# Kernel optimization log

Measured on AMD Instinct MI355X. Metric: run time of the kernel, lower is better.

The kernel has to match this reference:

```python
import jax, jax.numpy as jnp
import numpy as np
import math

EMBED_DIM = 1024
N_HEADS = 16
HEAD_DIM = EMBED_DIM // N_HEADS
NUM_FEATURES = 32
R_NODES = 2
EPS = 1e-06
C_CONST = 2.0 + EPS
CHUNK = 512


def setup_inputs() -> dict:
    key = jax.random.key(0)
    ks = jax.random.split(key, 8)
    B, T = 2, 4096
    x = jax.random.normal(ks[0], (B, T, EMBED_DIM), dtype=jnp.float32)
    w_qkv = jax.random.normal(ks[1], (3 * EMBED_DIM, EMBED_DIM), dtype=jnp.float32) * 0.02
    b_qkv = jnp.zeros((3 * EMBED_DIM,), dtype=jnp.float32)
    w_out = jax.random.normal(ks[2], (EMBED_DIM, EMBED_DIM), dtype=jnp.float32) * 0.02
    b_out = jnp.zeros((EMBED_DIM,), dtype=jnp.float32)
    omega = jax.random.normal(ks[3], (R_NODES, N_HEADS, HEAD_DIM, NUM_FEATURES), dtype=jnp.float32)
    nodes, weights = np.polynomial.laguerre.laggauss(R_NODES)
    quad_nodes = jnp.asarray(nodes, dtype=jnp.float32) / C_CONST
    quad_weights = jnp.asarray(weights, dtype=jnp.float32) / C_CONST
    return {"x": x, "w_qkv": w_qkv, "b_qkv": b_qkv, "w_out": w_out,
            "b_out": b_out, "omega": omega, "quad_nodes": quad_nodes,
            "quad_weights": quad_weights}


def _compute_features(z, omega, quad_nodes, quad_weights):
    # z: [B,H,T,D] -> fused features [B,H,T,R*M]
    R, M = omega.shape[0], omega.shape[-1]
    nrm = jnp.linalg.norm(z, axis=-1, keepdims=True)
    zn = z / jnp.maximum(nrm, 1e-12)  # F.normalize
    proj = jnp.einsum('bhtd,rhdm->rbhtm', zn, omega)
    inv_sqrt_m = 1.0 / math.sqrt(M)
    poly = (proj ** 2) * inv_sqrt_m
    s = quad_nodes.reshape(R, 1, 1, 1, 1)
    sqrt_2s = jnp.sqrt(2.0 * jnp.maximum(quad_nodes, 0.0)).reshape(R, 1, 1, 1, 1)
    exp_arg = jnp.clip(proj * sqrt_2s - s, -20.0, 20.0)
    prf = jnp.exp(exp_arg) * inv_sqrt_m
    sqw = jnp.sqrt(jnp.maximum(quad_weights, 0.0)).reshape(R, 1, 1, 1, 1)
    fused = poly * prf * sqw  # [R,B,H,T,M]
    B, H, T = z.shape[0], z.shape[1], z.shape[2]
    return jnp.transpose(fused, (1, 2, 3, 0, 4)).reshape(B, H, T, R * M)


def _forward(x, w_qkv, b_qkv, w_out, b_out, omega, quad_nodes, quad_weights):
    B, T, C = x.shape
    H, D = N_HEADS, HEAD_DIM
    qkv = x @ w_qkv.T + b_qkv  # [B,T,3C]
    q, k, v = jnp.split(qkv, 3, axis=-1)
    def to_bhtd(t):
        return jnp.transpose(t.reshape(B, T, H, D), (0, 2, 1, 3)).astype(jnp.float32)
    q, k, v = to_bhtd(q), to_bhtd(k), to_bhtd(v)
    qf = _compute_features(q, omega, quad_nodes, quad_weights)  # [B,H,T,F]
    kf = _compute_features(k, omega, quad_nodes, quad_weights)
    F_dim = qf.shape[-1]
    nc = T // CHUNK
    # chunked causal linear attention via scan over chunks
    def to_chunks(t):  # [B,H,T,...] -> [nc,B,H,CHUNK,...]
        new_shape = (t.shape[0], t.shape[1], nc, CHUNK) + t.shape[3:]
        return jnp.moveaxis(t.reshape(new_shape), 2, 0)
    qf_c, kf_c, v_c = to_chunks(qf), to_chunks(kf), to_chunks(v)

    kv0 = jnp.zeros((B, H, F_dim, D), dtype=jnp.float32)
    k0 = jnp.zeros((B, H, F_dim), dtype=jnp.float32)

    def step(carry, inp):
        kv_s, k_s = carry
        qc, kc, vc = inp
        kv_prod = jnp.einsum('bhtf,bhtd->bhtfd', kc, vc)
        kv_cum = jnp.cumsum(kv_prod, axis=2) + kv_s[:, :, None]
        k_cum = jnp.cumsum(kc, axis=2) + k_s[:, :, None]
        ctx = jnp.einsum('bhtf,bhtfd->bhtd', qc, kv_cum)
        den = jnp.maximum(jnp.einsum('bhtf,bhtf->bht', qc, k_cum), 1e-06)
        out_c = ctx / den[..., None]
        return (kv_cum[:, :, -1], k_cum[:, :, -1]), out_c

    _, out_chunks = jax.lax.scan(step, (kv0, k0), (qf_c, kf_c, v_c))
    out = jnp.moveaxis(out_chunks, 0, 2).reshape(B, H, T, D)  # [B,H,T,D]
    out = jnp.transpose(out, (0, 2, 1, 3)).reshape(B, T, C)
    return out @ w_out.T + b_out


def reference(x, w_qkv, b_qkv, w_out, b_out, omega, quad_nodes, quad_weights):
    return _forward(x, w_qkv, b_qkv, w_out, b_out, omega, quad_nodes, quad_weights)
```

## Files before the change

kernel.cpp:

```cpp
#include <hip/hip_runtime.h>
#include <math.h>

#define EMBED   1024
#define THREEC  3072
#define NH      16
#define HD      64
#define NFEAT   64
#define RN      2
#define MM_     32
#define B_      2
#define T_      4096
#define L_      64
#define NC_     64
#define BH_     32

typedef __attribute__((ext_vector_type(8))) short bf16x8;
typedef __attribute__((ext_vector_type(4))) float f32x4;

__device__ __forceinline__ float bf2f(short s) {
    unsigned u = ((unsigned)(unsigned short)s) << 16;
    return __builtin_bit_cast(float, u);
}
__device__ __forceinline__ short f2bf(float f) {
    unsigned u = __builtin_bit_cast(unsigned, f);
    u += 0x7fff + ((u >> 16) & 1);
    return (short)(u >> 16);
}
__device__ __forceinline__ void gload16(const short* g, short* l) {
    __builtin_amdgcn_global_load_lds(
        (const __attribute__((address_space(1))) void*)g,
        (__attribute__((address_space(3))) void*)l, 16, 0, 0);
}

#define NV_X   1048576
#define NV_WQ  393216
#define NV_WO  131072
#define NV_ALL (NV_X + NV_WQ + NV_WO)
__global__ __launch_bounds__(256) void prep_kernel(
    const float* __restrict__ x, const float* __restrict__ wq,
    const float* __restrict__ wo, const float* __restrict__ omega,
    short* __restrict__ xb, short* __restrict__ wqb, short* __restrict__ wob,
    short* __restrict__ omgH, short* __restrict__ omgL)
{
    int i = blockIdx.x * 256 + threadIdx.x;
    if (i < NV_ALL) {
        const float* src; short* dst; int k;
        if (i < NV_X)            { src = x;  dst = xb;  k = i; }
        else if (i < NV_X+NV_WQ) { src = wq; dst = wqb; k = i - NV_X; }
        else                     { src = wo; dst = wob; k = i - NV_X - NV_WQ; }
        const float4* p = (const float4*)src + (size_t)k * 2;
        float4 a = p[0], b = p[1];
        bf16x8 o = { f2bf(a.x), f2bf(a.y), f2bf(a.z), f2bf(a.w),
                     f2bf(b.x), f2bf(b.y), f2bf(b.z), f2bf(b.w) };
        *((bf16x8*)dst + k) = o;
    } else {
        int j = i - NV_ALL;
        if (j < NH * NFEAT * HD) {
            int d = j & 63;
            int f = (j >> 6) & 63;
            int h = j >> 12;
            int r = f >> 5, m = f & 31;
            float w = omega[(((size_t)(r * NH + h) * HD + d) * MM_) + m];
            short a = f2bf(w);
            omgH[j] = a;
            omgL[j] = f2bf(w - bf2f(a));
        }
    }
}

template<int OUTBF>
__global__ __launch_bounds__(256) void gemm_bf16(
    const short* __restrict__ A,
    const short* __restrict__ W,
    const float* __restrict__ bias,
    float* __restrict__ Cf, short* __restrict__ Cb,
    int M, int N, int K)
{
    __shared__ short lA[2][128 * 32];
    __shared__ short lB[2][128 * 32];
    const int tid  = threadIdx.x;
    const int bm   = blockIdx.y * 128;
    const int bn   = blockIdx.x * 128;
    const int lane = tid & 63;
    const int wave = tid >> 6;
    const int row0 = (wave >> 1) * 64;
    const int col0 = (wave & 1) * 64;
    const int lr   = lane & 15;
    const int kg8  = (lane >> 4) * 8;

    f32x4 acc[4][4] = {};

#define STAGE(buf, k0)                                                        \
    {                                                                         \
        _Pragma("unroll")                                                     \
        for (int i = 0; i < 2; ++i) {                                         \
            int idx = i * 256 + tid;                                          \
            int row = idx >> 2, kq = (idx & 3) * 8;                           \
            gload16(&A[(size_t)(bm + row) * K + (k0) + kq], &lA[buf][idx * 8]); \
            gload16(&W[(size_t)(bn + row) * K + (k0) + kq], &lB[buf][idx * 8]); \
        }                                                                     \
    }

    const int KT = K >> 5;
    STAGE(0, 0);
    __syncthreads();
    int cur = 0;
    for (int kt = 0; kt < KT; ++kt) {
        if (kt + 1 < KT) STAGE(cur ^ 1, (kt + 1) * 32);
        const short* As = lA[cur];
        const short* Bs = lB[cur];
        bf16x8 af[4], bfr[4];
        #pragma unroll
        for (int m = 0; m < 4; ++m)
            af[m] = *(const bf16x8*)&As[(row0 + m * 16 + lr) * 32 + kg8];
        #pragma unroll
        for (int n = 0; n < 4; ++n)
            bfr[n] = *(const bf16x8*)&Bs[(col0 + n * 16 + lr) * 32 + kg8];
        #pragma unroll
        for (int m = 0; m < 4; ++m)
            #pragma unroll
            for (int n = 0; n < 4; ++n)
                acc[m][n] = __builtin_amdgcn_mfma_f32_16x16x32_bf16(
                    af[m], bfr[n], acc[m][n], 0, 0, 0);
        __syncthreads();
        cur ^= 1;
    }
#undef STAGE

    #pragma unroll
    for (int n = 0; n < 4; ++n) {
        const int col = bn + col0 + n * 16 + (lane & 15);
        const float bvv = bias[col];
        #pragma unroll
        for (int m = 0; m < 4; ++m) {
            const int rbase = bm + row0 + m * 16 + (lane >> 4) * 4;
            #pragma unroll
            for (int j = 0; j < 4; ++j) {
                const float v = acc[m][n][j] + bvv;
                if (OUTBF) Cb[(size_t)(rbase + j) * N + col] = f2bf(v);
                else       Cf[(size_t)(rbase + j) * N + col] = v;
            }
        }
    }
}

__global__ __launch_bounds__(256) void features_chunk(
    const short* __restrict__ qkvb,
    const short* __restrict__ omgH,
    const short* __restrict__ omgL,
    const float* __restrict__ qn,
    const float* __restrict__ qw,
    short* __restrict__ qf,
    short* __restrict__ kf,
    float* __restrict__ cKV,
    float* __restrict__ cK)
{
    __shared__ short zq[64][72];
    __shared__ short zk[64][72];
    __shared__ short omh[64][72];
    __shared__ short oml[64][72];
    __shared__ float invn[2][64];

    const int tid   = threadIdx.x;
    const int chunk = blockIdx.x;
    const int bh    = chunk >> 6;
    const int c     = chunk & 63;
    const int b     = bh >> 4, h = bh & 15;
    const int t0    = c * 64;

    {
        const int row = tid >> 2;
        const int c0  = (tid & 3) * 16;
        const size_t zbase = ((size_t)(b * T_ + t0 + row)) * THREEC + h * HD + c0;
        const size_t obase = ((size_t)h * NFEAT + row) * HD + c0;
        *(bf16x8*)&zq[row][c0]      = *(const bf16x8*)&qkvb[zbase];
        *(bf16x8*)&zq[row][c0 + 8]  = *(const bf16x8*)&qkvb[zbase + 8];
        *(bf16x8*)&zk[row][c0]      = *(const bf16x8*)&qkvb[zbase + EMBED];
        *(bf16x8*)&zk[row][c0 + 8]  = *(const bf16x8*)&qkvb[zbase + EMBED + 8];
        *(bf16x8*)&omh[row][c0]     = *(const bf16x8*)&omgH[obase];
        *(bf16x8*)&omh[row][c0 + 8] = *(const bf16x8*)&omgH[obase + 8];
        *(bf16x8*)&oml[row][c0]     = *(const bf16x8*)&omgL[obase];
        *(bf16x8*)&oml[row][c0 + 8] = *(const bf16x8*)&omgL[obase + 8];
    }
    __syncthreads();

    {
        const int t = tid >> 2;
        const int q = tid & 3;
        #pragma unroll
        for (int p = 0; p < 2; ++p) {
            const short* Z = p ? &zk[t][q * 16] : &zq[t][q * 16];
            float ss = 0.0f;
            #pragma unroll
            for (int j = 0; j < 16; ++j) { float v = bf2f(Z[j]); ss += v * v; }
            ss += __shfl_xor(ss, 1, 64);
            ss += __shfl_xor(ss, 2, 64);
            if (q == 0) invn[p][t] = 1.0f / fmaxf(sqrtf(ss), 1e-12f);
        }
    }
    __syncthreads();

    const int wave = tid >> 6;
    const int lane = tid & 63;
    const int p    = wave >> 1;
    const int half = wave & 1;
    const short (*Z)[72] = p ? zk : zq;

    const float s0 = qn[0], s1 = qn[1];
    const float sq2s0 = sqrtf(2.0f * fmaxf(s0, 0.0f));
    const float sq2s1 = sqrtf(2.0f * fmaxf(s1, 0.0f));
    const float sc0 = sqrtf(fmaxf(qw[0], 0.0f)) * (1.0f / 32.0f);
    const float sc1 = sqrtf(fmaxf(qw[1], 0.0f)) * (1.0f / 32.0f);

    const int lr  = lane & 15;
    const int G   = lane >> 4;
    const int kg8 = G * 8;

    f32x4 acc[2][4] = {};
    #pragma unroll
    for (int kk = 0; kk < 2; ++kk) {
        bf16x8 a[2], bh8[4], bl8[4];
        #pragma unroll
        for (int m = 0; m < 2; ++m)
            a[m] = *(const bf16x8*)&Z[half * 32 + m * 16 + lr][kk * 32 + kg8];
        #pragma unroll
        for (int n = 0; n < 4; ++n) {
            bh8[n] = *(const bf16x8*)&omh[n * 16 + lr][kk * 32 + kg8];
            bl8[n] = *(const bf16x8*)&oml[n * 16 + lr][kk * 32 + kg8];
        }
        #pragma unroll
        for (int m = 0; m < 2; ++m)
            #pragma unroll
            for (int n = 0; n < 4; ++n) {
                acc[m][n] = __builtin_amdgcn_mfma_f32_16x16x32_bf16(
                    a[m], bh8[n], acc[m][n], 0, 0, 0);
                acc[m][n] = __builtin_amdgcn_mfma_f32_16x16x32_bf16(
                    a[m], bl8[n], acc[m][n], 0, 0, 0);
            }
    }
    __syncthreads();

    short (*kfT)[72] = zq;
    short (*vT)[72]  = zk;
    {
        short* dstbase = (p ? kf : qf) + ((size_t)bh * T_ + t0) * NFEAT;
        #pragma unroll
        for (int n = 0; n < 4; ++n) {
            const int f = n * 16 + lr;
            const float s_r   = (n < 2) ? s0 : s1;
            const float sq2s  = (n < 2) ? sq2s0 : sq2s1;
            const float scale = (n < 2) ? sc0 : sc1;
            #pragma unroll
            for (int m = 0; m < 2; ++m) {
                const int tb4 = half * 32 + m * 16 + G * 4;
                #pragma unroll
                for (int j = 0; j < 4; ++j) {
                    const int t = tb4 + j;
                    const float proj = acc[m][n][j] * invn[p][t];
                    const float arg = fminf(fmaxf(proj * sq2s - s_r, -20.0f), 20.0f);
                    const float val = proj * proj * __expf(arg) * scale;
                    const short vb  = f2bf(val);
                    dstbase[(size_t)t * NFEAT + f] = vb;
                    if (p == 1) kfT[f][t] = vb;
                }
            }
        }
    }
    {
        const int row = tid >> 2;
        const int c0  = (tid & 3) * 16;
        const short* vrow = qkvb + ((size_t)(b * T_ + t0 + row)) * THREEC
                          + 2 * EMBED + h * HD;
        bf16x8 v0 = *(const bf16x8*)&vrow[c0], v1 = *(const bf16x8*)&vrow[c0 + 8];
        #pragma unroll
        for (int j = 0; j < 8; ++j) {
            vT[c0 + j][row]     = v0[j];
            vT[c0 + 8 + j][row] = v1[j];
        }
    }
    __syncthreads();

    {
        bf16x8 a2[2], bv8[4][2];
        a2[0] = *(const bf16x8*)&kfT[wave * 16 + lr][kg8];
        a2[1] = *(const bf16x8*)&kfT[wave * 16 + lr][32 + kg8];
        #pragma unroll
        for (int n = 0; n < 4; ++n) {
            bv8[n][0] = *(const bf16x8*)&vT[n * 16 + lr][kg8];
            bv8[n][1] = *(const bf16x8*)&vT[n * 16 + lr][32 + kg8];
        }
        f32x4 sa[4] = {};
        #pragma unroll
        for (int n = 0; n < 4; ++n) {
            sa[n] = __builtin_amdgcn_mfma_f32_16x16x32_bf16(a2[0], bv8[n][0], sa[n], 0, 0, 0);
            sa[n] = __builtin_amdgcn_mfma_f32_16x16x32_bf16(a2[1], bv8[n][1], sa[n], 0, 0, 0);
        }
        float* base = cKV + (size_t)chunk * (NFEAT * HD);
        #pragma unroll
        for (int n = 0; n < 4; ++n) {
            float4 o; o.x = sa[n][0]; o.y = sa[n][1]; o.z = sa[n][2]; o.w = sa[n][3];
            *(float4*)&base[(n * 16 + lr) * NFEAT + wave * 16 + G * 4] = o;
        }
    }
    {
        const int f  = tid >> 2;
        const int tq = tid & 3;
        float s = 0.0f;
        #pragma unroll
        for (int j = 0; j < 16; ++j) s += bf2f(kfT[f][tq * 16 + j]);
        s += __shfl_xor(s, 1, 64);
        s += __shfl_xor(s, 2, 64);
        if (tq == 0) cK[(size_t)chunk * NFEAT + f] = s;
    }
}

__global__ __launch_bounds__(256) void prefix_scan(
    float* __restrict__ cKV, float* __restrict__ cK)
{
    const int bh  = blockIdx.x >> 2;
    const int sl  = blockIdx.x & 3;
    const int tid = threadIdx.x;
    float4* base = (float4*)(cKV + (size_t)bh * NC_ * (NFEAT * HD) + sl * 1024) + tid;
    float4 n0 = base[0];
    float4 n1 = base[1024];
    float4 pref; pref.x = pref.y = pref.z = pref.w = 0.0f;
    for (int c = 0; c < NC_; ++c) {
        float4 cur = n0;
        n0 = n1;
        if (c + 2 < NC_) n1 = base[(size_t)(c + 2) * 1024];
        else { n1.x = n1.y = n1.z = n1.w = 0.0f; }
        base[(size_t)c * 1024] = pref;
        pref.x += cur.x; pref.y += cur.y; pref.z += cur.z; pref.w += cur.w;
    }
    if (sl == 0 && tid < 64) {
        float* kb = cK + (size_t)bh * NC_ * NFEAT + tid;
        float m0 = kb[0];
        float m1 = kb[64];
        float p = 0.0f;
        for (int c = 0; c < NC_; ++c) {
            float cu = m0;
            m0 = m1;
            m1 = (c + 2 < NC_) ? kb[(size_t)(c + 2) * 64] : 0.0f;
            kb[(size_t)c * 64] = p;
            p += cu;
        }
    }
}

__global__ __launch_bounds__(256) void intra_mfma(
    const short* __restrict__ qf,
    const short* __restrict__ kf,
    const short* __restrict__ qkvb,
    const float* __restrict__ cKV,
    const float* __restrict__ cK,
    short* __restrict__ attnb)
{
    __shared__ short Qs[64][72];
    __shared__ short Ks[64][72];
    __shared__ short Vt[64][72];
    __shared__ short Pp[64][72];
    __shared__ short At[64][72];
    __shared__ float rs_l[64], qkp_l[64], cKp[64];

    const int tid = threadIdx.x;
    const int chunk = blockIdx.x;
    const int bh = chunk >> 6, c = chunk & 63;
    const int b = bh >> 4, h = bh & 15;
    const int t0 = c * L_;

    {
        const int row = tid >> 2;
        const int c0  = (tid & 3) * 16;
        const short* qrow = qf + ((size_t)bh * T_ + t0 + row) * NFEAT;
        const short* krow = kf + ((size_t)bh * T_ + t0 + row) * NFEAT;
        const short* vrow = qkvb + ((size_t)(b * T_ + t0 + row)) * THREEC + 2 * EMBED + h * HD;
        *(bf16x8*)&Qs[row][c0]     = *(const bf16x8*)&qrow[c0];
        *(bf16x8*)&Qs[row][c0 + 8] = *(const bf16x8*)&qrow[c0 + 8];
        *(bf16x8*)&Ks[row][c0]     = *(const bf16x8*)&krow[c0];
        *(bf16x8*)&Ks[row][c0 + 8] = *(const bf16x8*)&krow[c0 + 8];
        bf16x8 v0 = *(const bf16x8*)&vrow[c0], v1 = *(const bf16x8*)&vrow[c0 + 8];
        #pragma unroll
        for (int j = 0; j < 8; ++j) {
            Vt[c0 + j][row]     = v0[j];
            Vt[c0 + 8 + j][row] = v1[j];
        }
        const float* pbase = cKV + (size_t)chunk * (NFEAT * HD) + tid * 16;
        float4 p0 = *(const float4*)&pbase[0],  p1 = *(const float4*)&pbase[4];
        float4 p2 = *(const float4*)&pbase[8],  p3 = *(const float4*)&pbase[12];
        bf16x8 o0 = { f2bf(p0.x), f2bf(p0.y), f2bf(p0.z), f2bf(p0.w),
                      f2bf(p1.x), f2bf(p1.y), f2bf(p1.z), f2bf(p1.w) };
        bf16x8 o1 = { f2bf(p2.x), f2bf(p2.y), f2bf(p2.z), f2bf(p2.w),
                      f2bf(p3.x), f2bf(p3.y), f2bf(p3.z), f2bf(p3.w) };
        *(bf16x8*)&Pp[row][c0]     = o0;
        *(bf16x8*)&Pp[row][c0 + 8] = o1;
        if (tid < 64) cKp[tid] = cK[(size_t)chunk * NFEAT + tid];
    }
    __syncthreads();

    const int wave = tid >> 6;
    const int lane = tid & 63;
    const int lr   = lane & 15;
    const int kg   = (lane >> 4) * 8;
    const int r0   = wave * 16;

    bf16x8 aq[2];
    aq[0] = *(const bf16x8*)&Qs[r0 + lr][kg];
    aq[1] = *(const bf16x8*)&Qs[r0 + lr][32 + kg];
    f32x4 accA[4] = {};
    #pragma unroll
    for (int n = 0; n < 4; ++n) {
        accA[n] = __builtin_amdgcn_mfma_f32_16x16x32_bf16(
            aq[0], *(const bf16x8*)&Ks[n * 16 + lr][kg], accA[n], 0, 0, 0);
        accA[n] = __builtin_amdgcn_mfma_f32_16x16x32_bf16(
            aq[1], *(const bf16x8*)&Ks[n * 16 + lr][32 + kg], accA[n], 0, 0, 0);
    }
    float rsum[4] = {0.0f, 0.0f, 0.0f, 0.0f};
    #pragma unroll
    for (int n = 0; n < 4; ++n) {
        const int s = n * 16 + lr;
        #pragma unroll
        for (int j = 0; j < 4; ++j) {
            const int t = r0 + (lane >> 4) * 4 + j;
            const float a = (s <= t) ? accA[n][j] : 0.0f;
            rsum[j] += a;
            At[t][s] = f2bf(a);
        }
    }
    #pragma unroll
    for (int j = 0; j < 4; ++j) {
        rsum[j] += __shfl_xor(rsum[j], 1, 64);
        rsum[j] += __shfl_xor(rsum[j], 2, 64);
        rsum[j] += __shfl_xor(rsum[j], 4, 64);
        rsum[j] += __shfl_xor(rsum[j], 8, 64);
    }
    if (lr == 0) {
        #pragma unroll
        for (int j = 0; j < 4; ++j) rs_l[r0 + (lane >> 4) * 4 + j] = rsum[j];
    }

    {
        const int t  = tid >> 2;
        const int fq = (tid & 3) * 16;
        float s = 0.0f;
        #pragma unroll
        for (int j = 0; j < 16; ++j) s += bf2f(Qs[t][fq + j]) * cKp[fq + j];
        s += __shfl_xor(s, 1, 64);
        s += __shfl_xor(s, 2, 64);
        if ((tid & 3) == 0) qkp_l[t] = s;
    }
    __syncthreads();

    bf16x8 aa[2];
    aa[0] = *(const bf16x8*)&At[r0 + lr][kg];
    aa[1] = *(const bf16x8*)&At[r0 + lr][32 + kg];
    f32x4 acc[4] = {};
    #pragma unroll
    for (int n = 0; n < 4; ++n) {
        acc[n] = __builtin_amdgcn_mfma_f32_16x16x32_bf16(
            aa[0], *(const bf16x8*)&Vt[n * 16 + lr][kg], acc[n], 0, 0, 0);
        acc[n] = __builtin_amdgcn_mfma_f32_16x16x32_bf16(
            aa[1], *(const bf16x8*)&Vt[n * 16 + lr][32 + kg], acc[n], 0, 0, 0);
        acc[n] = __builtin_amdgcn_mfma_f32_16x16x32_bf16(
            aq[0], *(const bf16x8*)&Pp[n * 16 + lr][kg], acc[n], 0, 0, 0);
        acc[n] = __builtin_amdgcn_mfma_f32_16x16x32_bf16(
            aq[1], *(const bf16x8*)&Pp[n * 16 + lr][32 + kg], acc[n], 0, 0, 0);
    }

    float inv[4];
    #pragma unroll
    for (int j = 0; j < 4; ++j) {
        const int t = r0 + (lane >> 4) * 4 + j;
        inv[j] = 1.0f / fmaxf(rs_l[t] + qkp_l[t], 1e-6f);
    }
    #pragma unroll
    for (int n = 0; n < 4; ++n) {
        const int d = n * 16 + lr;
        #pragma unroll
        for (int j = 0; j < 4; ++j) {
            const int t = r0 + (lane >> 4) * 4 + j;
            attnb[((size_t)(b * T_ + t0 + t)) * EMBED + h * HD + d] =
                f2bf(acc[n][j] * inv[j]);
        }
    }
}

extern "C" void kernel_launch(void* const* d_in, const int* in_sizes, int n_in,
                              void* d_out, int out_size, void* d_ws, size_t ws_size,
                              hipStream_t stream)
{
    const float* x     = (const float*)d_in[0];
    const float* w_qkv = (const float*)d_in[1];
    const float* b_qkv = (const float*)d_in[2];
    const float* w_out = (const float*)d_in[3];
    const float* b_out = (const float*)d_in[4];
    const float* omega = (const float*)d_in[5];
    const float* qn    = (const float*)d_in[6];
    const float* qw    = (const float*)d_in[7];
    float* out = (float*)d_out;

    short* xb    = (short*)d_ws;
    short* wqb   = xb    + 8388608;
    short* wob   = wqb   + 3145728;
    short* qkvb  = wob   + 1048576;
    short* attnb = qkvb  + 25165824;
    short* omgH  = attnb + 8388608;
    short* omgL  = omgH  + 65536;
    short* qfb   = omgL  + 65536;
    short* kfb   = qfb   + 8388608;
    float* cKV   = (float*)(kfb + 8388608);
    float* cK    = cKV + 8388608;

    const int M = B_ * T_;

    prep_kernel<<<dim3((NV_ALL + 65536) / 256), 256, 0, stream>>>(
        x, w_qkv, w_out, omega, xb, wqb, wob, omgH, omgL);

    gemm_bf16<1><<<dim3(THREEC / 128, M / 128), 256, 0, stream>>>(
        xb, wqb, b_qkv, nullptr, qkvb, M, THREEC, EMBED);
    features_chunk<<<dim3(BH_ * NC_), 256, 0, stream>>>(
        qkvb, omgH, omgL, qn, qw, qfb, kfb, cKV, cK);
    prefix_scan<<<dim3(BH_ * 4), 256, 0, stream>>>(cKV, cK);
    intra_mfma<<<dim3(BH_ * NC_), 256, 0, stream>>>(qfb, kfb, qkvb, cKV, cK, attnb);
    gemm_bf16<0><<<dim3(EMBED / 128, M / 128), 256, 0, stream>>>(
        attnb, wob, b_out, out, nullptr, M, EMBED, EMBED);
}
```

Measured before the change: 170.7 us.

## Fuse intra-chunk attention into feature kernel and store chunk KV states in bf16

Intra-chunk causal attention (QK^T mask, A·V and row sums) now runs inside the features kernel, which already holds the Q/K features and V in shared memory. The partial context and row sums go to global memory, and the inter-chunk kernel only applies the prefix state and normalises. This drops the kf write and reread plus the V reload. Per-chunk KV states and their prefix sums are now stored in bf16 instead of fp32, halving that traffic at some precision cost in the prefix accumulation. An extra bf16 ctx buffer is written and read, which adds traffic and rounds the intra-chunk context once more.

```diff
diff --git a/kernel.cpp b/kernel.cpp
--- a/kernel.cpp
+++ b/kernel.cpp
@@ -15,6 +15,7 @@
 #define BH_     32
 
 typedef __attribute__((ext_vector_type(8))) short bf16x8;
+typedef __attribute__((ext_vector_type(4))) short bf16x4;
 typedef __attribute__((ext_vector_type(4))) float f32x4;
 
 __device__ __forceinline__ float bf2f(short s) {
@@ -144,15 +145,16 @@
     }
 }
 
-__global__ __launch_bounds__(256) void features_chunk(
+__global__ __launch_bounds__(256) void feat_fused(
     const short* __restrict__ qkvb,
     const short* __restrict__ omgH,
     const short* __restrict__ omgL,
     const float* __restrict__ qn,
     const float* __restrict__ qw,
     short* __restrict__ qf,
-    short* __restrict__ kf,
-    float* __restrict__ cKV,
+    short* __restrict__ ctxb,
+    float* __restrict__ rs_g,
+    short* __restrict__ cKVb,
     float* __restrict__ cK)
 {
     __shared__ short zq[64][72];
@@ -160,6 +162,7 @@
     __shared__ short omh[64][72];
     __shared__ short oml[64][72];
     __shared__ float invn[2][64];
+    __shared__ float rs_l[64];
 
     const int tid   = threadIdx.x;
     const int chunk = blockIdx.x;
@@ -242,8 +245,9 @@
 
     short (*kfT)[72] = zq;
     short (*vT)[72]  = zk;
-    {
-        short* dstbase = (p ? kf : qf) + ((size_t)bh * T_ + t0) * NFEAT;
+    short (*Qrm)[72] = omh;
+    short (*Krm)[72] = oml;
+    {
         #pragma unroll
         for (int n = 0; n < 4; ++n) {
             const int f = n * 16 + lr;
@@ -260,8 +264,8 @@
                     const float arg = fminf(fmaxf(proj * sq2s - s_r, -20.0f), 20.0f);
                     const float val = proj * proj * __expf(arg) * scale;
                     const short vb  = f2bf(val);
-                    dstbase[(size_t)t * NFEAT + f] = vb;
-                    if (p == 1) kfT[f][t] = vb;
+                    if (p == 0) { Qrm[t][f] = vb; }
+                    else        { kfT[f][t] = vb; Krm[t][f] = vb; }
                 }
             }
         }
@@ -280,26 +284,67 @@
     }
     __syncthreads();
 
-    {
-        bf16x8 a2[2], bv8[4][2];
+    const int r0 = wave * 16;
+
+    {
+        const int row = tid >> 2;
+        const int c0  = (tid & 3) * 16;
+        short* dst = qf + ((size_t)bh * T_ + t0 + row) * NFEAT;
+        *(bf16x8*)&dst[c0]     = *(const bf16x8*)&Qrm[row][c0];
+        *(bf16x8*)&dst[c0 + 8] = *(const bf16x8*)&Qrm[row][c0 + 8];
+    }
+    bf16x8 aqq[2];
+    aqq[0] = *(const bf16x8*)&Qrm[r0 + lr][kg8];
+    aqq[1] = *(const bf16x8*)&Qrm[r0 + lr][32 + kg8];
+    f32x4 accA[4] = {};
+    #pragma unroll
+    for (int n = 0; n < 4; ++n) {
+        accA[n] = __builtin_amdgcn_mfma_f32_16x16x32_bf16(
+            aqq[0], *(const bf16x8*)&Krm[n * 16 + lr][kg8], accA[n], 0, 0, 0);
+        accA[n] = __builtin_amdgcn_mfma_f32_16x16x32_bf16(
+            aqq[1], *(const bf16x8*)&Krm[n * 16 + lr][32 + kg8], accA[n], 0, 0, 0);
+    }
+    {
+        float rsum[4] = {0.0f, 0.0f, 0.0f, 0.0f};
+        #pragma unroll
+        for (int n = 0; n < 4; ++n) {
+            const int s = n * 16 + lr;
+            #pragma unroll
+            for (int j = 0; j < 4; ++j) {
+                const int t = r0 + G * 4 + j;
+                if (s <= t) rsum[j] += accA[n][j];
+            }
+        }
+        #pragma unroll
+        for (int j = 0; j < 4; ++j) {
+            rsum[j] += __shfl_xor(rsum[j], 1, 64);
+            rsum[j] += __shfl_xor(rsum[j], 2, 64);
+            rsum[j] += __shfl_xor(rsum[j], 4, 64);
+            rsum[j] += __shfl_xor(rsum[j], 8, 64);
+        }
+        if (lr == 0) {
+            #pragma unroll
+            for (int j = 0; j < 4; ++j) rs_l[r0 + G * 4 + j] = rsum[j];
+        }
+    }
+    {
+        bf16x8 a2[2];
         a2[0] = *(const bf16x8*)&kfT[wave * 16 + lr][kg8];
         a2[1] = *(const bf16x8*)&kfT[wave * 16 + lr][32 + kg8];
-        #pragma unroll
-        for (int n = 0; n < 4; ++n) {
-            bv8[n][0] = *(const bf16x8*)&vT[n * 16 + lr][kg8];
-            bv8[n][1] = *(const bf16x8*)&vT[n * 16 + lr][32 + kg8];
-        }
         f32x4 sa[4] = {};
         #pragma unroll
         for (int n = 0; n < 4; ++n) {
-            sa[n] = __builtin_amdgcn_mfma_f32_16x16x32_bf16(a2[0], bv8[n][0], sa[n], 0, 0, 0);
-            sa[n] = __builtin_amdgcn_mfma_f32_16x16x32_bf16(a2[1], bv8[n][1], sa[n], 0, 0, 0);
-        }
-        float* base = cKV + (size_t)chunk * (NFEAT * HD);
-        #pragma unroll
-        for (int n = 0; n < 4; ++n) {
-            float4 o; o.x = sa[n][0]; o.y = sa[n][1]; o.z = sa[n][2]; o.w = sa[n][3];
-            *(float4*)&base[(n * 16 + lr) * NFEAT + wave * 16 + G * 4] = o;
+            sa[n] = __builtin_amdgcn_mfma_f32_16x16x32_bf16(
+                a2[0], *(const bf16x8*)&vT[n * 16 + lr][kg8], sa[n], 0, 0, 0);
+            sa[n] = __builtin_amdgcn_mfma_f32_16x16x32_bf16(
+                a2[1], *(const bf16x8*)&vT[n * 16 + lr][32 + kg8], sa[n], 0, 0, 0);
+        }
+        short* basep = cKVb + (size_t)chunk * (NFEAT * HD);
+        #pragma unroll
+        for (int n = 0; n < 4; ++n) {
+            bf16x4 o = { f2bf(sa[n][0]), f2bf(sa[n][1]),
+                         f2bf(sa[n][2]), f2bf(sa[n][3]) };
+            *(bf16x4*)&basep[(n * 16 + lr) * NFEAT + wave * 16 + G * 4] = o;
         }
     }
     {
@@ -312,25 +357,64 @@
         s += __shfl_xor(s, 2, 64);
         if (tq == 0) cK[(size_t)chunk * NFEAT + f] = s;
     }
+    __syncthreads();
+
+    short (*At)[72] = oml;
+    #pragma unroll
+    for (int n = 0; n < 4; ++n) {
+        const int s = n * 16 + lr;
+        #pragma unroll
+        for (int j = 0; j < 4; ++j) {
+            const int t = r0 + G * 4 + j;
+            At[t][s] = f2bf((s <= t) ? accA[n][j] : 0.0f);
+        }
+    }
+    __syncthreads();
+
+    {
+        bf16x8 aa[2];
+        aa[0] = *(const bf16x8*)&At[r0 + lr][kg8];
+        aa[1] = *(const bf16x8*)&At[r0 + lr][32 + kg8];
+        f32x4 a2[4] = {};
+        #pragma unroll
+        for (int n = 0; n < 4; ++n) {
+            a2[n] = __builtin_amdgcn_mfma_f32_16x16x32_bf16(
+                aa[0], *(const bf16x8*)&vT[n * 16 + lr][kg8], a2[n], 0, 0, 0);
+            a2[n] = __builtin_amdgcn_mfma_f32_16x16x32_bf16(
+                aa[1], *(const bf16x8*)&vT[n * 16 + lr][32 + kg8], a2[n], 0, 0, 0);
+        }
+        #pragma unroll
+        for (int n = 0; n < 4; ++n) {
+            const int d = n * 16 + lr;
+            #pragma unroll
+            for (int j = 0; j < 4; ++j) {
+                const int t = r0 + G * 4 + j;
+                ctxb[((size_t)bh * T_ + t0 + t) * NFEAT + d] = f2bf(a2[n][j]);
+            }
+        }
+    }
+    if (tid < 64) rs_g[(size_t)bh * T_ + t0 + tid] = rs_l[tid];
 }
 
 __global__ __launch_bounds__(256) void prefix_scan(
-    float* __restrict__ cKV, float* __restrict__ cK)
+    short* __restrict__ cKVb, float* __restrict__ cK)
 {
     const int bh  = blockIdx.x >> 2;
     const int sl  = blockIdx.x & 3;
     const int tid = threadIdx.x;
-    float4* base = (float4*)(cKV + (size_t)bh * NC_ * (NFEAT * HD) + sl * 1024) + tid;
-    float4 n0 = base[0];
-    float4 n1 = base[1024];
-    float4 pref; pref.x = pref.y = pref.z = pref.w = 0.0f;
+    short* base = cKVb + (size_t)bh * NC_ * (NFEAT * HD) + sl * 1024 + tid * 4;
+    bf16x4 n0 = *(const bf16x4*)(base);
+    bf16x4 n1 = *(const bf16x4*)(base + 4096);
+    float pref[4] = {0.0f, 0.0f, 0.0f, 0.0f};
     for (int c = 0; c < NC_; ++c) {
-        float4 cur = n0;
+        bf16x4 cur = n0;
         n0 = n1;
-        if (c + 2 < NC_) n1 = base[(size_t)(c + 2) * 1024];
-        else { n1.x = n1.y = n1.z = n1.w = 0.0f; }
-        base[(size_t)c * 1024] = pref;
-        pref.x += cur.x; pref.y += cur.y; pref.z += cur.z; pref.w += cur.w;
+        if (c + 2 < NC_) n1 = *(const bf16x4*)(base + (size_t)(c + 2) * 4096);
+        else { n1[0] = 0; n1[1] = 0; n1[2] = 0; n1[3] = 0; }
+        bf16x4 o = { f2bf(pref[0]), f2bf(pref[1]), f2bf(pref[2]), f2bf(pref[3]) };
+        *(bf16x4*)(base + (size_t)c * 4096) = o;
+        pref[0] += bf2f(cur[0]); pref[1] += bf2f(cur[1]);
+        pref[2] += bf2f(cur[2]); pref[3] += bf2f(cur[3]);
     }
     if (sl == 0 && tid < 64) {
         float* kb = cK + (size_t)bh * NC_ * NFEAT + tid;
@@ -347,139 +431,86 @@
     }
 }
 
-__global__ __launch_bounds__(256) void intra_mfma(
+__global__ __launch_bounds__(256) void inter_attn(
     const short* __restrict__ qf,
-    const short* __restrict__ kf,
-    const short* __restrict__ qkvb,
-    const float* __restrict__ cKV,
-    const float* __restrict__ cK,
+    const short* __restrict__ ctxb,
+    const float* __restrict__ rs_g,
+    const short* __restrict__ cKVp,
+    const float* __restrict__ cKp_g,
     short* __restrict__ attnb)
 {
-    __shared__ short Qs[64][72];
-    __shared__ short Ks[64][72];
-    __shared__ short Vt[64][72];
+    __shared__ short Q[64][72];
     __shared__ short Pp[64][72];
-    __shared__ short At[64][72];
-    __shared__ float rs_l[64], qkp_l[64], cKp[64];
+    __shared__ float cKp[64], rs[64], qkp_l[64];
 
     const int tid = threadIdx.x;
     const int chunk = blockIdx.x;
     const int bh = chunk >> 6, c = chunk & 63;
     const int b = bh >> 4, h = bh & 15;
-    const int t0 = c * L_;
+    const int t0 = c * 64;
 
     {
         const int row = tid >> 2;
         const int c0  = (tid & 3) * 16;
-        const short* qrow = qf + ((size_t)bh * T_ + t0 + row) * NFEAT;
-        const short* krow = kf + ((size_t)bh * T_ + t0 + row) * NFEAT;
-        const short* vrow = qkvb + ((size_t)(b * T_ + t0 + row)) * THREEC + 2 * EMBED + h * HD;
-        *(bf16x8*)&Qs[row][c0]     = *(const bf16x8*)&qrow[c0];
-        *(bf16x8*)&Qs[row][c0 + 8] = *(const bf16x8*)&qrow[c0 + 8];
-        *(bf16x8*)&Ks[row][c0]     = *(const bf16x8*)&krow[c0];
-        *(bf16x8*)&Ks[row][c0 + 8] = *(const bf16x8*)&krow[c0 + 8];
-        bf16x8 v0 = *(const bf16x8*)&vrow[c0], v1 = *(const bf16x8*)&vrow[c0 + 8];
-        #pragma unroll
-        for (int j = 0; j < 8; ++j) {
-            Vt[c0 + j][row]     = v0[j];
-            Vt[c0 + 8 + j][row] = v1[j];
-        }
-        const float* pbase = cKV + (size_t)chunk * (NFEAT * HD) + tid * 16;
-        float4 p0 = *(const float4*)&pbase[0],  p1 = *(const float4*)&pbase[4];
-        float4 p2 = *(const float4*)&pbase[8],  p3 = *(const float4*)&pbase[12];
-        bf16x8 o0 = { f2bf(p0.x), f2bf(p0.y), f2bf(p0.z), f2bf(p0.w),
-                      f2bf(p1.x), f2bf(p1.y), f2bf(p1.z), f2bf(p1.w) };
-        bf16x8 o1 = { f2bf(p2.x), f2bf(p2.y), f2bf(p2.z), f2bf(p2.w),
-                      f2bf(p3.x), f2bf(p3.y), f2bf(p3.z), f2bf(p3.w) };
-        *(bf16x8*)&Pp[row][c0]     = o0;
-        *(bf16x8*)&Pp[row][c0 + 8] = o1;
-        if (tid < 64) cKp[tid] = cK[(size_t)chunk * NFEAT + tid];
-    }
-    __syncthreads();
-
-    const int wave = tid >> 6;
-    const int lane = tid & 63;
-    const int lr   = lane & 15;
-    const int kg   = (lane >> 4) * 8;
-    const int r0   = wave * 16;
-
-    bf16x8 aq[2];
-    aq[0] = *(const bf16x8*)&Qs[r0 + lr][kg];
-    aq[1] = *(const bf16x8*)&Qs[r0 + lr][32 + kg];
-    f32x4 accA[4] = {};
-    #pragma unroll
-    for (int n = 0; n < 4; ++n) {
-        accA[n] = __builtin_amdgcn_mfma_f32_16x16x32_bf16(
-            aq[0], *(const bf16x8*)&Ks[n * 16 + lr][kg], accA[n], 0, 0, 0);
-        accA[n] = __builtin_amdgcn_mfma_f32_16x16x32_bf16(
-            aq[1], *(const bf16x8*)&Ks[n * 16 + lr][32 + kg], accA[n], 0, 0, 0);
-    }
-    float rsum[4] = {0.0f, 0.0f, 0.0f, 0.0f};
-    #pragma unroll
-    for (int n = 0; n < 4; ++n) {
-        const int s = n * 16 + lr;
-        #pragma unroll
-        for (int j = 0; j < 4; ++j) {
-            const int t = r0 + (lane >> 4) * 4 + j;
-            const float a = (s <= t) ? accA[n][j] : 0.0f;
-            rsum[j] += a;
-            At[t][s] = f2bf(a);
-        }
-    }
-    #pragma unroll
-    for (int j = 0; j < 4; ++j) {
-        rsum[j] += __shfl_xor(rsum[j], 1, 64);
-        rsum[j] += __shfl_xor(rsum[j], 2, 64);
-        rsum[j] += __shfl_xor(rsum[j], 4, 64);
-        rsum[j] += __shfl_xor(rsum[j], 8, 64);
-    }
-    if (lr == 0) {
-        #pragma unroll
-        for (int j = 0; j < 4; ++j) rs_l[r0 + (lane >> 4) * 4 + j] = rsum[j];
-    }
+        const short* qrow = qf   + ((size_t)bh * T_ + t0 + row) * NFEAT;
+        const short* prow = cKVp + (size_t)chunk * (NFEAT * HD) + row * NFEAT;
+        *(bf16x8*)&Q[row][c0]      = *(const bf16x8*)&qrow[c0];
+        *(bf16x8*)&Q[row][c0 + 8]  = *(const bf16x8*)&qrow[c0 + 8];
+        *(bf16x8*)&Pp[row][c0]     = *(const bf16x8*)&prow[c0];
+        *(bf16x8*)&Pp[row][c0 + 8] = *(const bf16x8*)&prow[c0 + 8];
+        if (tid < 64) {
+            cKp[tid] = cKp_g[(size_t)chunk * NFEAT + tid];
+            rs[tid]  = rs_g[(size_t)bh * T_ + t0 + tid];
+        }
+    }
+    __syncthreads();
 
     {
         const int t  = tid >> 2;
         const int fq = (tid & 3) * 16;
         float s = 0.0f;
         #pragma unroll
-        for (int j = 0; j < 16; ++j) s += bf2f(Qs[t][fq + j]) * cKp[fq + j];
+        for (int j = 0; j < 16; ++j) s += bf2f(Q[t][fq + j]) * cKp[fq + j];
         s += __shfl_xor(s, 1, 64);
         s += __shfl_xor(s, 2, 64);
         if ((tid & 3) == 0) qkp_l[t] = s;
     }
-    __syncthreads();
-
-    bf16x8 aa[2];
-    aa[0] = *(const bf16x8*)&At[r0 + lr][kg];
-    aa[1] = *(const bf16x8*)&At[r0 + lr][32 + kg];
+
+    const int wave = tid >> 6;
+    const int lane = tid & 63;
+    const int lr = lane & 15;
+    const int G  = lane >> 4;
+    const int kg = G * 8;
+    const int r0 = wave * 16;
+
+    bf16x8 aq[2];
+    aq[0] = *(const bf16x8*)&Q[r0 + lr][kg];
+    aq[1] = *(const bf16x8*)&Q[r0 + lr][32 + kg];
     f32x4 acc[4] = {};
     #pragma unroll
     for (int n = 0; n < 4; ++n) {
-        acc[n] = __builtin_amdgcn_mfma_f32_16x16x32_bf16(
-            aa[0], *(const bf16x8*)&Vt[n * 16 + lr][kg], acc[n], 0, 0, 0);
-        acc[n] = __builtin_amdgcn_mfma_f32_16x16x32_bf16(
-            aa[1], *(const bf16x8*)&Vt[n * 16 + lr][32 + kg], acc[n], 0, 0, 0);
         acc[n] = __builtin_amdgcn_mfma_f32_16x16x32_bf16(
             aq[0], *(const bf16x8*)&Pp[n * 16 + lr][kg], acc[n], 0, 0, 0);
         acc[n] = __builtin_amdgcn_mfma_f32_16x16x32_bf16(
             aq[1], *(const bf16x8*)&Pp[n * 16 + lr][32 + kg], acc[n], 0, 0, 0);
     }
+    __syncthreads();
 
     float inv[4];
     #pragma unroll
     for (int j = 0; j < 4; ++j) {
-        const int t = r0 + (lane >> 4) * 4 + j;
-        inv[j] = 1.0f / fmaxf(rs_l[t] + qkp_l[t], 1e-6f);
+        const int t = r0 + G * 4 + j;
+        inv[j] = 1.0f / fmaxf(rs[t] + qkp_l[t], 1e-6f);
     }
     #pragma unroll
     for (int n = 0; n < 4; ++n) {
         const int d = n * 16 + lr;
         #pragma unroll
         for (int j = 0; j < 4; ++j) {
-            const int t = r0 + (lane >> 4) * 4 + j;
+            const int t = r0 + G * 4 + j;
+            const float ctx = bf2f(ctxb[((size_t)bh * T_ + t0 + t) * NFEAT + d]);
             attnb[((size_t)(b * T_ + t0 + t)) * EMBED + h * HD + d] =
-                f2bf(acc[n][j] * inv[j]);
+                f2bf((ctx + acc[n][j]) * inv[j]);
         }
     }
 }
@@ -506,9 +537,10 @@
     short* omgH  = attnb + 8388608;
     short* omgL  = omgH  + 65536;
     short* qfb   = omgL  + 65536;
-    short* kfb   = qfb   + 8388608;
-    float* cKV   = (float*)(kfb + 8388608);
-    float* cK    = cKV + 8388608;
+    short* ctxb  = qfb   + 8388608;
+    short* cKVb  = ctxb  + 8388608;
+    float* cK    = (float*)(cKVb + 8388608);
+    float* rs_g  = cK + 131072;
 
     const int M = B_ * T_;
 
@@ -517,10 +549,11 @@
 
     gemm_bf16<1><<<dim3(THREEC / 128, M / 128), 256, 0, stream>>>(
         xb, wqb, b_qkv, nullptr, qkvb, M, THREEC, EMBED);
-    features_chunk<<<dim3(BH_ * NC_), 256, 0, stream>>>(
-        qkvb, omgH, omgL, qn, qw, qfb, kfb, cKV, cK);
-    prefix_scan<<<dim3(BH_ * 4), 256, 0, stream>>>(cKV, cK);
-    intra_mfma<<<dim3(BH_ * NC_), 256, 0, stream>>>(qfb, kfb, qkvb, cKV, cK, attnb);
+    feat_fused<<<dim3(BH_ * NC_), 256, 0, stream>>>(
+        qkvb, omgH, omgL, qn, qw, qfb, ctxb, rs_g, cKVb, cK);
+    prefix_scan<<<dim3(BH_ * 4), 256, 0, stream>>>(cKVb, cK);
+    inter_attn<<<dim3(BH_ * NC_), 256, 0, stream>>>(
+        qfb, ctxb, rs_g, cKVb, cK, attnb);
     gemm_bf16<0><<<dim3(EMBED / 128, M / 128), 256, 0, stream>>>(
         attnb, wob, b_out, out, nullptr, M, EMBED, EMBED);
 }
```

New measurement: 170.4 us. No clear change (-0.2%).
